# Performance work log

Hardware: AMD Instinct MI355X
Metric: run time of the kernel (lower is better)

Reference implementation:

```python
import jax, jax.numpy as jnp
import numpy as np

B = 16384          # batch
NS = 26            # sparse features
ND = 13            # dense features
V = 100000         # vocab per sparse feature
E = 16             # embedding size
H = 400            # dnn hidden
DNN_IN = NS * E + ND  # 429


def setup_inputs() -> dict:
    key = jax.random.key(0)
    ks = jax.random.split(key, 12)
    X_sparse = jax.random.randint(ks[0], (B, NS), 0, V, dtype=jnp.int32)
    X_dense = jax.random.normal(ks[1], (B, ND), dtype=jnp.float32)
    # stacked per-feature embedding tables: [NS, V, dim]
    emb1 = jax.random.normal(ks[2], (NS, V, 1), dtype=jnp.float32) * 1e-4
    emb2 = jax.random.normal(ks[3], (NS, V, E), dtype=jnp.float32) * 1e-4
    lin_weight = jax.random.normal(ks[4], (ND, 1), dtype=jnp.float32) * 1e-4
    bias = jnp.zeros((1,), dtype=jnp.float32)
    W0 = jax.random.normal(ks[5], (DNN_IN, H), dtype=jnp.float32) * 1e-4
    b0 = jnp.zeros((H,), dtype=jnp.float32)
    W1 = jax.random.normal(ks[6], (H, H), dtype=jnp.float32) * 1e-4
    b1 = jnp.zeros((H,), dtype=jnp.float32)
    W2 = jax.random.normal(ks[7], (H, H), dtype=jnp.float32) * 1e-4
    b2 = jnp.zeros((H,), dtype=jnp.float32)
    W_out = jax.random.normal(ks[8], (H, 1), dtype=jnp.float32) * 1e-4
    return {"X_sparse": X_sparse, "X_dense": X_dense, "emb1": emb1, "emb2": emb2,
            "lin_weight": lin_weight, "bias": bias, "W0": W0, "b0": b0,
            "W1": W1, "b1": b1, "W2": W2, "b2": b2, "W_out": W_out}


def reference(X_sparse, X_dense, emb1, emb2, lin_weight, bias, W0, b0, W1, b1, W2, b2, W_out):
    fidx = jnp.arange(NS)[None, :]            # [1, NS] feature indices
    # ---- FM linear term ----
    e1 = emb1[fidx, X_sparse][..., 0]          # [B, NS] per-feature scalar embeddings
    linear_sparse = jnp.sum(e1, axis=-1, keepdims=True)            # [B, 1]
    linear_dense = X_dense @ lin_weight                            # [B, 1]
    logit = linear_sparse + linear_dense
    # ---- FM second-order cross term ----
    e2 = emb2[fidx, X_sparse]                  # [B, NS, E]
    square_of_sum = jnp.square(jnp.sum(e2, axis=1))                # [B, E]
    sum_of_square = jnp.sum(jnp.square(e2), axis=1)                # [B, E]
    cross = 0.5 * jnp.sum(square_of_sum - sum_of_square, axis=-1, keepdims=True)
    logit = logit + cross
    # ---- DNN (dropout p=0 -> identity) ----
    dnn_in = jnp.concatenate([e2.reshape(e2.shape[0], -1), X_dense], axis=-1)  # [B, 429]
    h = jax.nn.relu(dnn_in @ W0 + b0)
    h = jax.nn.relu(h @ W1 + b1)
    h = jax.nn.relu(h @ W2 + b2)
    logit = logit + h @ W_out
    return logit + bias
```

## Files before the change

### kernel.cpp

```cpp
#include <hip/hip_runtime.h>
#include <hip/hip_bf16.h>

#define B_     16384
#define NS_    26
#define ND_    13
#define V_     100000
#define H_     400
#define NP     448
#define MT     64
#define ASTR   456
#define WCHB   (448 * 64)
#define WQTR   (112 * 64)

#define ACT_OFF   0
#define WBUF_OFF  (MT * ASTR)
#define FMV_OFF   (WBUF_OFF + 2 * WCHB)
#define DOT_OFF   (FMV_OFF + 256)
#define LDSB      (DOT_OFF + 256)

#define WAIT_VM7  0x0F77
#define WAIT_VM0  0x0F70

#define SC_A1   2097152.0f
#define SC_A2   2147483648.0f
#define SC_F0   0.125f
#define SC_F1   0.25f
#define SC_G    1.1368683772161603e-13f

typedef float f32x4 __attribute__((ext_vector_type(4)));

__device__ __forceinline__ unsigned char f2fp8(float v) {
  int pk = __builtin_amdgcn_cvt_pk_fp8_f32(v, v, 0, false);
  return (unsigned char)(pk & 0xff);
}

__global__ __launch_bounds__(256) void prep_w(
    const float* __restrict__ W0, const float* __restrict__ W1,
    const float* __restrict__ W2, const float* __restrict__ b0,
    const float* __restrict__ b1, const float* __restrict__ b2,
    const float* __restrict__ Wout,
    unsigned char* __restrict__ W0t, unsigned char* __restrict__ W1t,
    unsigned char* __restrict__ W2t, float* __restrict__ b0p,
    float* __restrict__ b1p, float* __restrict__ b2p,
    float* __restrict__ woutp) {
  const int blk = blockIdx.x;
  const int tid = threadIdx.x;
  if (blk < 147) {
    const int layer = blk / 49;
    const int t = blk - layer * 49;
    const int k0 = (t / 7) * 64, n0 = (t - (t / 7) * 7) * 64;
    const float* W = (layer == 0) ? W0 : (layer == 1) ? W1 : W2;
    unsigned char* Wt = (layer == 0) ? W0t : (layer == 1) ? W1t : W2t;
    const int Kdim = (layer == 0) ? 429 : 400;
    __shared__ float tile[64][65];
#pragma unroll
    for (int p = 0; p < 16; ++p) {
      int kk = p * 4 + (tid >> 6);
      int k = k0 + kk;
      int n = n0 + (tid & 63);
      float v = (k < Kdim && n < H_) ? W[k * H_ + n] : 0.f;
      tile[kk][tid & 63] = v;
    }
    __syncthreads();
#pragma unroll
    for (int p = 0; p < 4; ++p) {
      int nn = p * 16 + (tid >> 4);
      int n = n0 + nn;
      int k4 = (tid & 15) * 4;
      float sc[4];
#pragma unroll
      for (int i = 0; i < 4; ++i) {
        int kabs = k0 + k4 + i;
        sc[i] = (layer == 0 && kabs >= 416) ? 262144.0f : 4096.0f;
      }
      float v0 = tile[k4 + 0][nn] * sc[0];
      float v1 = tile[k4 + 1][nn] * sc[1];
      float v2 = tile[k4 + 2][nn] * sc[2];
      float v3 = tile[k4 + 3][nn] * sc[3];
      int w = __builtin_amdgcn_cvt_pk_fp8_f32(v0, v1, 0, false);
      w = __builtin_amdgcn_cvt_pk_fp8_f32(v2, v3, w, true);
      *(unsigned int*)(Wt + (size_t)n * NP + k0 + k4) = (unsigned int)w;
    }
  } else {
    for (int it = 0; it < 7; ++it) {
      int j = it * 256 + tid;
      if (j < NP)              b0p[j]          = (j < H_) ? b0[j] * SC_A1 : 0.f;
      else if (j < 2 * NP)     b1p[j - NP]     = (j - NP < H_) ? b1[j - NP] * SC_A2 : 0.f;
      else if (j < 3 * NP)     b2p[j - 2*NP]   = (j - 2*NP < H_) ? b2[j - 2*NP] : 0.f;
      else if (j < 4 * NP)     woutp[j - 3*NP] = (j - 3*NP < H_) ? Wout[j - 3*NP] : 0.f;
    }
  }
}

__device__ __forceinline__ void stage_w_chunk(
    const unsigned char* __restrict__ Wt, int kt, unsigned char* wb,
    int wave, int lane) {
  const unsigned char* wrow = Wt + (size_t)(wave * 112) * NP + kt * 64;
  unsigned char* lbase = wb + wave * WQTR;
#pragma unroll
  for (int i = 0; i < 7; ++i) {
    int s = i * 64 + lane;
    int nl = s >> 2;
    int g = (s & 3) ^ ((nl >> 1) & 3);
    const unsigned char* gp = wrow + (size_t)nl * NP + g * 16;
    unsigned char* lp = lbase + (size_t)(i * 64) * 16;
    __builtin_amdgcn_global_load_lds(
        (const __attribute__((address_space(1))) unsigned int*)gp,
        (__attribute__((address_space(3))) unsigned int*)lp, 16, 0, 0);
  }
}

__global__ __launch_bounds__(256, 1) void fused_all(
    const int* __restrict__ Xs, const float* __restrict__ Xd,
    const float* __restrict__ emb1, const float* __restrict__ emb2,
    const float* __restrict__ linw, const float* __restrict__ bias,
    const unsigned char* __restrict__ W0t, const unsigned char* __restrict__ W1t,
    const unsigned char* __restrict__ W2t,
    const float* __restrict__ b0p, const float* __restrict__ b1p,
    const float* __restrict__ b2p, const float* __restrict__ woutp,
    float* __restrict__ out) {
  extern __shared__ char smem[];
  unsigned char* act  = (unsigned char*)(smem + ACT_OFF);
  unsigned char* wbuf = (unsigned char*)(smem + WBUF_OFF);
  float* fmv  = (float*)(smem + FMV_OFF);
  float* dotv = (float*)(smem + DOT_OFF);

  const int tid  = threadIdx.x;
  const int wave = tid >> 6;
  const int lane = tid & 63;
  const int quad = lane >> 4;
  const int l16  = lane & 15;
  const int r0   = blockIdx.x * MT;

  stage_w_chunk(W0t, 0, wbuf, wave, lane);

  {
    if (tid < 64) dotv[tid] = 0.f;
    const int r   = lane >> 2;
    const int t4  = lane & 3;
    const int row = wave * 16 + r;
    const int gr  = r0 + row;
    const int* xs = Xs + gr * NS_;

    f32x4 sum = {0.f, 0.f, 0.f, 0.f}, sq = {0.f, 0.f, 0.f, 0.f};
#pragma unroll
    for (int f = 0; f < NS_; ++f) {
      int idx = xs[f];
      f32x4 v = *(const f32x4*)(emb2 + ((size_t)f * V_ + idx) * 16 + t4 * 4);
      sum += v;
      sq  += v * v;
      int pk = __builtin_amdgcn_cvt_pk_fp8_f32(v[0] * 4096.f, v[1] * 4096.f, 0, false);
      pk = __builtin_amdgcn_cvt_pk_fp8_f32(v[2] * 4096.f, v[3] * 4096.f, pk, true);
      *(unsigned int*)(act + row * ASTR + f * 16 + t4 * 4) = (unsigned int)pk;
    }

    float lin = 0.f;
    for (int f = t4; f < NS_; f += 4)
      lin += emb1[(size_t)f * V_ + xs[f]];

    for (int e = 416 + t4; e < NP; e += 4) act[row * ASTR + e] = 0;
    for (int e = t4; e < ND_; e += 4) {
      float xd = Xd[gr * ND_ + e];
      lin += xd * linw[e];
      act[row * ASTR + 416 + e] = f2fp8(xd * 64.f);
    }

    f32x4 c4 = sum * sum - sq;
    float fm = 0.5f * (c4[0] + c4[1] + c4[2] + c4[3]) + lin;
    fm += __shfl_xor(fm, 1, 64);
    fm += __shfl_xor(fm, 2, 64);
    if (t4 == 0) fmv[row] = fm + bias[0];
  }

  __syncthreads();

  const unsigned char* Wl[3] = {W0t, W1t, W2t};

  for (int layer = 0; layer < 3; ++layer) {
    const unsigned char* Wt = Wl[layer];
    const unsigned char* wq = wbuf + wave * WQTR;
    f32x4 acc[4][7] = {};

    for (int kt = 0; kt < 7; ++kt) {
      if (kt < 6) {
        stage_w_chunk(Wt, kt + 1, wbuf + ((kt + 1) & 1) * WCHB, wave, lane);
        __builtin_amdgcn_s_waitcnt(WAIT_VM7);
      } else {
        __builtin_amdgcn_s_waitcnt(WAIT_VM0);
      }
      __builtin_amdgcn_sched_barrier(0);
      const unsigned char* wb = wq + (kt & 1) * WCHB;

#pragma unroll
      for (int h = 0; h < 2; ++h) {
        long long av[4];
#pragma unroll
        for (int mt = 0; mt < 4; ++mt)
          av[mt] = *(const long long*)(act + (mt * 16 + l16) * ASTR + kt * 64 + h * 32 + quad * 8);
#pragma unroll
        for (int nt = 0; nt < 7; ++nt) {
          int nl = nt * 16 + l16;
          int sw = (2 * h + (quad >> 1)) ^ ((nl >> 1) & 3);
          long long bv = *(const long long*)(wb + nl * 64 + sw * 16 + (quad & 1) * 8);
#pragma unroll
          for (int mt = 0; mt < 4; ++mt)
            acc[mt][nt] = __builtin_amdgcn_mfma_f32_16x16x32_fp8_fp8(av[mt], bv, acc[mt][nt], 0, 0, 0);
        }
      }
    }

    if (layer < 2) stage_w_chunk(Wl[layer + 1], 0, wbuf, wave, lane);

    __syncthreads();

    if (layer < 2) {
      const float fs = (layer == 0) ? SC_F0 : SC_F1;
      const float* bl = (layer == 0) ? b0p : b1p;
#pragma unroll
      for (int nt = 0; nt < 7; ++nt) {
        int col = wave * 112 + nt * 16 + l16;
        float bz = bl[col];
#pragma unroll
        for (int mt = 0; mt < 4; ++mt) {
#pragma unroll
          for (int r = 0; r < 4; ++r) {
            float v = acc[mt][nt][r] * fs + bz;
            v = v > 0.f ? v : 0.f;
            act[(mt * 16 + quad * 4 + r) * ASTR + col] = f2fp8(v);
          }
        }
      }
    } else {
      float wsum[4][4] = {};
#pragma unroll
      for (int nt = 0; nt < 7; ++nt) {
        int col = wave * 112 + nt * 16 + l16;
        float bz = b2p[col];
        float wv = woutp[col];
#pragma unroll
        for (int mt = 0; mt < 4; ++mt) {
#pragma unroll
          for (int r = 0; r < 4; ++r) {
            float v = acc[mt][nt][r] * SC_G + bz;
            v = v > 0.f ? v : 0.f;
            wsum[mt][r] += v * wv;
          }
        }
      }
#pragma unroll
      for (int mt = 0; mt < 4; ++mt) {
#pragma unroll
        for (int r = 0; r < 4; ++r) {
          float s = wsum[mt][r];
          s += __shfl_xor(s, 1, 64);
          s += __shfl_xor(s, 2, 64);
          s += __shfl_xor(s, 4, 64);
          s += __shfl_xor(s, 8, 64);
          if (l16 == 0) atomicAdd(&dotv[mt * 16 + quad * 4 + r], s);
        }
      }
    }
    __syncthreads();
  }

  if (tid < 64) out[r0 + tid] = fmv[tid] + dotv[tid];
}

extern "C" void kernel_launch(void* const* d_in, const int* in_sizes, int n_in,
                              void* d_out, int out_size, void* d_ws, size_t ws_size,
                              hipStream_t stream) {
  const int*   Xs   = (const int*)d_in[0];
  const float* Xd   = (const float*)d_in[1];
  const float* emb1 = (const float*)d_in[2];
  const float* emb2 = (const float*)d_in[3];
  const float* linw = (const float*)d_in[4];
  const float* bias = (const float*)d_in[5];
  const float* W0   = (const float*)d_in[6];
  const float* b0   = (const float*)d_in[7];
  const float* W1   = (const float*)d_in[8];
  const float* b1   = (const float*)d_in[9];
  const float* W2   = (const float*)d_in[10];
  const float* b2   = (const float*)d_in[11];
  const float* Wout = (const float*)d_in[12];
  float* out = (float*)d_out;

  char* ws = (char*)d_ws;
  const size_t WSZ = (size_t)NP * NP;
  unsigned char* W0t = (unsigned char*)(ws);
  unsigned char* W1t = (unsigned char*)(ws + WSZ);
  unsigned char* W2t = (unsigned char*)(ws + 2 * WSZ);
  float* b0p   = (float*)(ws + 3 * WSZ);
  float* b1p   = (float*)(ws + 3 * WSZ + 1792);
  float* b2p   = (float*)(ws + 3 * WSZ + 2 * 1792);
  float* woutp = (float*)(ws + 3 * WSZ + 3 * 1792);

  (void)hipFuncSetAttribute((const void*)fused_all,
                            hipFuncAttributeMaxDynamicSharedMemorySize, LDSB);

  prep_w<<<148, 256, 0, stream>>>(W0, W1, W2, b0, b1, b2, Wout,
                                  W0t, W1t, W2t, b0p, b1p, b2p, woutp);

  fused_all<<<B_ / MT, 256, LDSB, stream>>>(
      Xs, Xd, emb1, emb2, linw, bias, W0t, W1t, W2t,
      b0p, b1p, b2p, woutp, out);
}
```

Measured before the change: 276.3 us.

## Move embedding gather into high-occupancy prep kernel, stage activations via workspace

Measured after the change: 270.5 us. -2.1%, faster.

```diff
diff --git a/kernel.cpp b/kernel.cpp
--- a/kernel.cpp
+++ b/kernel.cpp
@@ -14,9 +14,10 @@
 
 #define ACT_OFF   0
 #define WBUF_OFF  (MT * ASTR)
-#define FMV_OFF   (WBUF_OFF + 2 * WCHB)
-#define DOT_OFF   (FMV_OFF + 256)
+#define DOT_OFF   (WBUF_OFF + 2 * WCHB)
 #define LDSB      (DOT_OFF + 256)
+
+#define PREP_LDS  16640
 
 #define WAIT_VM7  0x0F77
 #define WAIT_VM0  0x0F70
@@ -34,17 +35,23 @@
   return (unsigned char)(pk & 0xff);
 }
 
-__global__ __launch_bounds__(256) void prep_w(
-    const float* __restrict__ W0, const float* __restrict__ W1,
-    const float* __restrict__ W2, const float* __restrict__ b0,
-    const float* __restrict__ b1, const float* __restrict__ b2,
+__global__ __launch_bounds__(256, 8) void gather_prep(
+    const int* __restrict__ Xs, const float* __restrict__ Xd,
+    const float* __restrict__ emb1, const float* __restrict__ emb2,
+    const float* __restrict__ linw, const float* __restrict__ bias,
+    const float* __restrict__ W0, const float* __restrict__ b0,
+    const float* __restrict__ W1, const float* __restrict__ b1,
+    const float* __restrict__ W2, const float* __restrict__ b2,
     const float* __restrict__ Wout,
     unsigned char* __restrict__ W0t, unsigned char* __restrict__ W1t,
-    unsigned char* __restrict__ W2t, float* __restrict__ b0p,
-    float* __restrict__ b1p, float* __restrict__ b2p,
-    float* __restrict__ woutp) {
+    unsigned char* __restrict__ W2t,
+    float* __restrict__ b0p, float* __restrict__ b1p,
+    float* __restrict__ b2p, float* __restrict__ woutp,
+    unsigned char* __restrict__ actw, float* __restrict__ fmw) {
+  extern __shared__ char smem[];
   const int blk = blockIdx.x;
   const int tid = threadIdx.x;
+
   if (blk < 147) {
     const int layer = blk / 49;
     const int t = blk - layer * 49;
@@ -52,7 +59,7 @@
     const float* W = (layer == 0) ? W0 : (layer == 1) ? W1 : W2;
     unsigned char* Wt = (layer == 0) ? W0t : (layer == 1) ? W1t : W2t;
     const int Kdim = (layer == 0) ? 429 : 400;
-    __shared__ float tile[64][65];
+    float (*tile)[65] = (float (*)[65])smem;
 #pragma unroll
     for (int p = 0; p < 16; ++p) {
       int kk = p * 4 + (tid >> 6);
@@ -81,7 +88,10 @@
       w = __builtin_amdgcn_cvt_pk_fp8_f32(v2, v3, w, true);
       *(unsigned int*)(Wt + (size_t)n * NP + k0 + k4) = (unsigned int)w;
     }
-  } else {
+    return;
+  }
+  if (blk == 147) {
+#pragma unroll
     for (int it = 0; it < 7; ++it) {
       int j = it * 256 + tid;
       if (j < NP)              b0p[j]          = (j < H_) ? b0[j] * SC_A1 : 0.f;
@@ -89,7 +99,61 @@
       else if (j < 3 * NP)     b2p[j - 2*NP]   = (j - 2*NP < H_) ? b2[j - 2*NP] : 0.f;
       else if (j < 4 * NP)     woutp[j - 3*NP] = (j - 3*NP < H_) ? Wout[j - 3*NP] : 0.f;
     }
-  }
+    return;
+  }
+
+  const int g   = blk - 148;
+  const int rh  = tid >> 5;
+  const int t   = tid & 31;
+  const int t4  = t & 3;
+  const int fo  = t >> 2;
+  const int row = g * 8 + rh;
+  const int* xs = Xs + row * NS_;
+  unsigned char* arow = actw + (size_t)row * NP;
+
+  f32x4 sum = {0.f, 0.f, 0.f, 0.f}, sq = {0.f, 0.f, 0.f, 0.f};
+#pragma unroll
+  for (int j = 0; j < 4; ++j) {
+    int f = fo + j * 8;
+    if (f < NS_) {
+      int idx = xs[f];
+      f32x4 v = *(const f32x4*)(emb2 + ((size_t)f * V_ + idx) * 16 + t4 * 4);
+      sum += v;
+      sq  += v * v;
+      int pk = __builtin_amdgcn_cvt_pk_fp8_f32(v[0] * 4096.f, v[1] * 4096.f, 0, false);
+      pk = __builtin_amdgcn_cvt_pk_fp8_f32(v[2] * 4096.f, v[3] * 4096.f, pk, true);
+      *(unsigned int*)(arow + f * 16 + t4 * 4) = (unsigned int)pk;
+    }
+  }
+
+  float lin = 0.f;
+  if (t < NS_) lin = emb1[(size_t)t * V_ + xs[t]];
+  unsigned char dv = 0;
+  if (t < ND_) {
+    float xd = Xd[row * ND_ + t];
+    lin += xd * linw[t];
+    dv = f2fp8(xd * 64.f);
+  }
+  arow[416 + t] = dv;
+
+#pragma unroll
+  for (int m = 4; m <= 16; m <<= 1) {
+#pragma unroll
+    for (int i = 0; i < 4; ++i) {
+      sum[i] += __shfl_xor(sum[i], m, 64);
+      sq[i]  += __shfl_xor(sq[i],  m, 64);
+    }
+  }
+  f32x4 c4 = sum * sum - sq;
+  float cross = 0.5f * (c4[0] + c4[1] + c4[2] + c4[3]);
+  cross += __shfl_xor(cross, 1, 64);
+  cross += __shfl_xor(cross, 2, 64);
+  lin += __shfl_xor(lin, 1, 64);
+  lin += __shfl_xor(lin, 2, 64);
+  lin += __shfl_xor(lin, 4, 64);
+  lin += __shfl_xor(lin, 8, 64);
+  lin += __shfl_xor(lin, 16, 64);
+  if (t == 0) fmw[row] = cross + lin + bias[0];
 }
 
 __device__ __forceinline__ void stage_w_chunk(
@@ -110,19 +174,16 @@
   }
 }
 
-__global__ __launch_bounds__(256, 1) void fused_all(
-    const int* __restrict__ Xs, const float* __restrict__ Xd,
-    const float* __restrict__ emb1, const float* __restrict__ emb2,
-    const float* __restrict__ linw, const float* __restrict__ bias,
+__global__ __launch_bounds__(256, 1) void gemm_all(
     const unsigned char* __restrict__ W0t, const unsigned char* __restrict__ W1t,
     const unsigned char* __restrict__ W2t,
     const float* __restrict__ b0p, const float* __restrict__ b1p,
     const float* __restrict__ b2p, const float* __restrict__ woutp,
+    const unsigned char* __restrict__ actw, const float* __restrict__ fmw,
     float* __restrict__ out) {
   extern __shared__ char smem[];
   unsigned char* act  = (unsigned char*)(smem + ACT_OFF);
   unsigned char* wbuf = (unsigned char*)(smem + WBUF_OFF);
-  float* fmv  = (float*)(smem + FMV_OFF);
   float* dotv = (float*)(smem + DOT_OFF);
 
   const int tid  = threadIdx.x;
@@ -134,42 +195,15 @@
 
   stage_w_chunk(W0t, 0, wbuf, wave, lane);
 
-  {
-    if (tid < 64) dotv[tid] = 0.f;
-    const int r   = lane >> 2;
-    const int t4  = lane & 3;
-    const int row = wave * 16 + r;
-    const int gr  = r0 + row;
-    const int* xs = Xs + gr * NS_;
-
-    f32x4 sum = {0.f, 0.f, 0.f, 0.f}, sq = {0.f, 0.f, 0.f, 0.f};
-#pragma unroll
-    for (int f = 0; f < NS_; ++f) {
-      int idx = xs[f];
-      f32x4 v = *(const f32x4*)(emb2 + ((size_t)f * V_ + idx) * 16 + t4 * 4);
-      sum += v;
-      sq  += v * v;
-      int pk = __builtin_amdgcn_cvt_pk_fp8_f32(v[0] * 4096.f, v[1] * 4096.f, 0, false);
-      pk = __builtin_amdgcn_cvt_pk_fp8_f32(v[2] * 4096.f, v[3] * 4096.f, pk, true);
-      *(unsigned int*)(act + row * ASTR + f * 16 + t4 * 4) = (unsigned int)pk;
-    }
-
-    float lin = 0.f;
-    for (int f = t4; f < NS_; f += 4)
-      lin += emb1[(size_t)f * V_ + xs[f]];
-
-    for (int e = 416 + t4; e < NP; e += 4) act[row * ASTR + e] = 0;
-    for (int e = t4; e < ND_; e += 4) {
-      float xd = Xd[gr * ND_ + e];
-      lin += xd * linw[e];
-      act[row * ASTR + 416 + e] = f2fp8(xd * 64.f);
-    }
-
-    f32x4 c4 = sum * sum - sq;
-    float fm = 0.5f * (c4[0] + c4[1] + c4[2] + c4[3]) + lin;
-    fm += __shfl_xor(fm, 1, 64);
-    fm += __shfl_xor(fm, 2, 64);
-    if (t4 == 0) fmv[row] = fm + bias[0];
+  if (tid < MT) dotv[tid] = 0.f;
+
+#pragma unroll
+  for (int it = 0; it < 14; ++it) {
+    int c = it * 256 + tid;
+    int row = c / 56;
+    int off = c - row * 56;
+    long long v = *(const long long*)(actw + (size_t)(r0 + row) * NP + off * 8);
+    *(long long*)(act + row * ASTR + off * 8) = v;
   }
 
   __syncthreads();
@@ -263,7 +297,7 @@
     __syncthreads();
   }
 
-  if (tid < 64) out[r0 + tid] = fmv[tid] + dotv[tid];
+  if (tid < MT) out[r0 + tid] = fmw[r0 + tid] + dotv[tid];
 }
 
 extern "C" void kernel_launch(void* const* d_in, const int* in_sizes, int n_in,
@@ -293,14 +327,16 @@
   float* b1p   = (float*)(ws + 3 * WSZ + 1792);
   float* b2p   = (float*)(ws + 3 * WSZ + 2 * 1792);
   float* woutp = (float*)(ws + 3 * WSZ + 3 * 1792);
-
-  (void)hipFuncSetAttribute((const void*)fused_all,
+  unsigned char* actw = (unsigned char*)(ws + 3 * WSZ + 4 * 1792);
+  float* fmw = (float*)(ws + 3 * WSZ + 4 * 1792 + (size_t)B_ * NP);
+
+  (void)hipFuncSetAttribute((const void*)gemm_all,
                             hipFuncAttributeMaxDynamicSharedMemorySize, LDSB);
 
-  prep_w<<<148, 256, 0, stream>>>(W0, W1, W2, b0, b1, b2, Wout,
-                                  W0t, W1t, W2t, b0p, b1p, b2p, woutp);
-
-  fused_all<<<B_ / MT, 256, LDSB, stream>>>(
-      Xs, Xd, emb1, emb2, linw, bias, W0t, W1t, W2t,
-      b0p, b1p, b2p, woutp, out);
-}
+  gather_prep<<<148 + B_ / 8, 256, PREP_LDS, stream>>>(
+      Xs, Xd, emb1, emb2, linw, bias, W0, b0, W1, b1, W2, b2, Wout,
+      W0t, W1t, W2t, b0p, b1p, b2p, woutp, actw, fmw);
+
+  gemm_all<<<B_ / MT, 256, LDSB, stream>>>(
+      W0t, W1t, W2t, b0p, b1p, b2p, woutp, actw, fmw, out);
+}
```
